# Kernel optimization log

Hardware: AMD Instinct MI355X
Metric: run time of the kernel (lower is better)

The kernel has to match this reference:

```python
import jax, jax.numpy as jnp
import numpy as np

EPS = 1e-9


def _feature_map(x, W, b):
    # nn.Linear: x @ W.T + b, then concat[exp(z), exp(-z)] on last dim
    z = jnp.einsum('bnd,ed->bne', x, W) + b
    return jnp.concatenate([jnp.exp(z), jnp.exp(-z)], axis=-1)  # [b, n, 2d]


def setup_inputs() -> dict:
    key = jax.random.key(0)
    ks = jax.random.split(key, 6)
    b, n, d = 4, 4096, 64
    s = 1.0 / np.sqrt(d)
    hidden = jax.random.normal(ks[0], (b, n, d), dtype=jnp.float32)
    # Hedgehog init is identity + zero bias; add tiny noise so grads are generic
    eye = jnp.eye(d, dtype=jnp.float32)
    Wq_mlp = eye + 0.02 * jax.random.normal(ks[1], (d, d), dtype=jnp.float32)
    Wk_mlp = eye + 0.02 * jax.random.normal(ks[2], (d, d), dtype=jnp.float32)
    bq_mlp = jnp.zeros((d,), dtype=jnp.float32)
    bk_mlp = jnp.zeros((d,), dtype=jnp.float32)
    Wq_base = s * jax.random.normal(ks[3], (d, d), dtype=jnp.float32)
    Wk_base = s * jax.random.normal(ks[4], (d, d), dtype=jnp.float32)
    return {"hidden_states": hidden, "Wq_mlp": Wq_mlp, "bq_mlp": bq_mlp,
            "Wk_mlp": Wk_mlp, "bk_mlp": bk_mlp,
            "Wq_base": Wq_base, "Wk_base": Wk_base}


def reference(hidden_states, Wq_mlp, bq_mlp, Wk_mlp, bk_mlp, Wq_base, Wk_base):
    d = hidden_states.shape[-1]
    # frozen base attention -> true_attn [b, n, n]
    qb = jnp.einsum('bnd,ed->bne', hidden_states, Wq_base)
    kb = jnp.einsum('bnd,ed->bne', hidden_states, Wk_base)
    true_attn = jax.nn.softmax(
        jnp.einsum('bmd,bnd->bmn', qb, kb) / jnp.sqrt(jnp.float32(d)), axis=-1)
    # hedgehog feature maps -> [b, n, 2d]
    q = _feature_map(hidden_states, Wq_mlp, bq_mlp)
    k = _feature_map(hidden_states, Wk_mlp, bk_mlp)
    # quadratic scores + softmax (note: linear-attention form is NOT used here)
    scores = jnp.einsum('bmd,bnd->bmn', q, k)
    pred_attn = jax.nn.softmax(scores, axis=-1)
    # soft-label cross entropy (KD loss)
    loss = jnp.mean(jnp.sum(-true_attn * jnp.log(pred_attn + EPS), axis=-1))
    return (loss, pred_attn, true_attn)
```

## Files before the change

kernel.cpp:

```cpp
#include <hip/hip_runtime.h>
#include <hip/hip_bf16.h>
#include <math.h>


#define B 4
#define N 4096
#define D 64
#define NROWS (B * N)
#define ATTN_ELEMS ((size_t)B * N * N)
#define FSTAT_BASE 12582912

typedef __attribute__((ext_vector_type(8))) short short8;
typedef __attribute__((ext_vector_type(4))) float float4v;

typedef unsigned short ushort_t;

__device__ __forceinline__ float fast_exp(float x) { return __expf(x); }
__device__ __forceinline__ float fast_log(float x) { return __logf(x); }

__device__ __forceinline__ void split_bf16(float x, ushort_t& hi, ushort_t& lo) {
  __hip_bfloat16 h = __float2bfloat16(x);
  float r = x - __bfloat162float(h);
  __hip_bfloat16 l = __float2bfloat16(r);
  hi = *(ushort_t*)&h;
  lo = *(ushort_t*)&l;
}

__device__ __forceinline__ void gload_lds16(const ushort_t* g, ushort_t* l) {
  __builtin_amdgcn_global_load_lds(
      (const __attribute__((address_space(1))) unsigned int*)g,
      (__attribute__((address_space(3))) unsigned int*)l, 16, 0, 0);
}

__device__ __forceinline__ float block_reduce(float v, bool is_max, float* red) {
#pragma unroll
  for (int o = 32; o > 0; o >>= 1) {
    float other = __shfl_down(v, o);
    v = is_max ? fmaxf(v, other) : (v + other);
  }
  int w = threadIdx.x >> 6;
  __syncthreads();
  if ((threadIdx.x & 63) == 0) red[w] = v;
  __syncthreads();
  return is_max ? fmaxf(fmaxf(red[0], red[1]), fmaxf(red[2], red[3]))
                : (red[0] + red[1] + red[2] + red[3]);
}

#define PR 32

__global__ __launch_bounds__(256, 2) void proj_kernel(
    const float* __restrict__ hidden,
    const float* __restrict__ Wq_mlp, const float* __restrict__ bq_mlp,
    const float* __restrict__ Wk_mlp, const float* __restrict__ bk_mlp,
    const float* __restrict__ Wq_base, const float* __restrict__ Wk_base,
    ushort_t* __restrict__ ws) {
  ushort_t* qbh = ws;
  ushort_t* qbl = ws + 1048576;
  ushort_t* kbh = ws + 2097152;
  ushort_t* kbl = ws + 3145728;
  ushort_t* qfh = ws + 4194304;
  ushort_t* qfl = ws + 6291456;
  ushort_t* kfh = ws + 8388608;
  ushort_t* kfl = ws + 10485760;

  __shared__ float wt[4][64 * 64];
  __shared__ float hs[PR][64];

  const int tid = threadIdx.x;
  const int r0 = blockIdx.x * PR;

  {
    const float* Wm[4] = {Wq_base, Wk_base, Wq_mlp, Wk_mlp};
#pragma unroll
    for (int m = 0; m < 4; ++m)
      for (int idx = tid; idx < 4096; idx += 256) {
        const int e = idx >> 6, d = idx & 63;
        wt[m][d * 64 + (e ^ (d & 31))] = Wm[m][idx];
      }
  }
  for (int idx = tid; idx < PR * 64; idx += 256)
    hs[idx >> 6][idx & 63] = hidden[(size_t)r0 * 64 + idx];
  __syncthreads();

  const int e = tid & 63;
  const int g0 = (tid >> 6) * (PR / 4);

  float aqb[PR / 4], akb[PR / 4], zq[PR / 4], zk[PR / 4];
  const float bq = bq_mlp[e], bk = bk_mlp[e];
#pragma unroll
  for (int g = 0; g < PR / 4; ++g) {
    aqb[g] = 0.f; akb[g] = 0.f; zq[g] = bq; zk[g] = bk;
  }

#pragma unroll 8
  for (int d = 0; d < 64; ++d) {
    const int wi = d * 64 + (e ^ (d & 31));
    const float w0 = wt[0][wi];
    const float w1 = wt[1][wi];
    const float w2 = wt[2][wi];
    const float w3 = wt[3][wi];
#pragma unroll
    for (int g = 0; g < PR / 4; ++g) {
      const float hd = hs[g0 + g][d];
      aqb[g] += hd * w0;
      akb[g] += hd * w1;
      zq[g] += hd * w2;
      zk[g] += hd * w3;
    }
  }

#pragma unroll
  for (int g = 0; g < PR / 4; ++g) {
    const int row = r0 + g0 + g;
    const size_t rb = (size_t)row * D + e;
    const size_t rf = (size_t)row * 2 * D + e;
    ushort_t hi, lo;
    split_bf16(aqb[g], hi, lo);        qbh[rb] = hi; qbl[rb] = lo;
    split_bf16(akb[g], hi, lo);        kbh[rb] = hi; kbl[rb] = lo;
    split_bf16(expf(zq[g]), hi, lo);   qfh[rf] = hi; qfl[rf] = lo;
    split_bf16(expf(-zq[g]), hi, lo);  qfh[rf + D] = hi; qfl[rf + D] = lo;
    split_bf16(expf(zk[g]), hi, lo);   kfh[rf] = hi; kfl[rf] = lo;
    split_bf16(expf(-zk[g]), hi, lo);  kfh[rf + D] = hi; kfl[rf + D] = lo;
  }
}

__global__ __launch_bounds__(256) void stats_kernel(
    const ushort_t* __restrict__ ws, float* __restrict__ fst) {
  const ushort_t* qbh = ws;
  const ushort_t* qbl = ws + 1048576;
  const ushort_t* kbh = ws + 2097152;
  const ushort_t* kbl = ws + 3145728;
  const ushort_t* qfh = ws + 4194304;
  const ushort_t* qfl = ws + 6291456;
  const ushort_t* kfh = ws + 8388608;
  const ushort_t* kfl = ws + 10485760;

  float* mt_ = fst;
  float* ist_ = fst + 16384;
  float* mp_ = fst + 32768;
  float* isp_ = fst + 49152;

  __shared__ ushort_t sbh[128 * 64];
  __shared__ ushort_t sbl[128 * 64];
  __shared__ ushort_t sfh[128 * 128];
  __shared__ ushort_t sfl[128 * 128];

  const int bid0 = blockIdx.x;
  const int bid = (bid0 & 7) * 32 + (bid0 >> 3);
  const int bt = bid >> 6;
  const int m0 = (bid & 63) * 64;
  const int tid = threadIdx.x;
  const int w = tid >> 6;
  const int lane = tid & 63;
  const int fr = lane & 15;
  const int quad = lane >> 4;
  const size_t rowb = (size_t)bt * N;

  const size_t ar = rowb + m0 + w * 16 + fr;
  short8 ath[2], atl[2], aph[4], apl[4];
#pragma unroll
  for (int kk = 0; kk < 2; ++kk) {
    ath[kk] = *(const short8*)&qbh[ar * 64 + kk * 32 + quad * 8];
    atl[kk] = *(const short8*)&qbl[ar * 64 + kk * 32 + quad * 8];
  }
#pragma unroll
  for (int kk = 0; kk < 4; ++kk) {
    aph[kk] = *(const short8*)&qfh[ar * 128 + kk * 32 + quad * 8];
    apl[kk] = *(const short8*)&qfl[ar * 128 + kk * 32 + quad * 8];
  }

  const int sr8 = lane >> 3, su8 = (lane & 7) ^ (lane >> 3);
  const int r4 = lane >> 4, u16 = lane & 15;

  float m_t[4], s_t[4], m_p[4], s_p[4];
#pragma unroll
  for (int r = 0; r < 4; ++r) {
    m_t[r] = -INFINITY; s_t[r] = 0.f;
    m_p[r] = -INFINITY; s_p[r] = 0.f;
  }

  for (int c = 0; c < 32; ++c) {
    const int n0 = c * 128;
    __syncthreads();
#pragma unroll
    for (int j = 0; j < 4; ++j) {
      const int g = j * 4 + w;
      const size_t grow = rowb + n0 + g * 8 + sr8;
      gload_lds16(kbh + grow * 64 + su8 * 8, &sbh[g * 512]);
      gload_lds16(kbl + grow * 64 + su8 * 8, &sbl[g * 512]);
    }
#pragma unroll
    for (int j = 0; j < 8; ++j) {
      const int g = j * 4 + w;
      const int su = u16 ^ ((g & 1) * 4 + r4);
      const size_t grow = rowb + n0 + g * 4 + r4;
      gload_lds16(kfh + grow * 128 + su * 8, &sfh[g * 512]);
      gload_lds16(kfl + grow * 128 + su * 8, &sfl[g * 512]);
    }
    __syncthreads();

    float4v acct[8];
#pragma unroll
    for (int tn = 0; tn < 8; ++tn) acct[tn] = (float4v)0.f;
#pragma unroll
    for (int tn = 0; tn < 8; ++tn) {
      const int brow = tn * 16 + fr;
#pragma unroll
      for (int kk = 0; kk < 2; ++kk) {
        const int u = ((kk * 4 + quad) ^ (fr & 7)) * 8;
        short8 bh = *(const short8*)&sbh[brow * 64 + u];
        short8 bl = *(const short8*)&sbl[brow * 64 + u];
        acct[tn] = __builtin_amdgcn_mfma_f32_16x16x32_bf16(ath[kk], bh, acct[tn], 0, 0, 0);
        acct[tn] = __builtin_amdgcn_mfma_f32_16x16x32_bf16(ath[kk], bl, acct[tn], 0, 0, 0);
        acct[tn] = __builtin_amdgcn_mfma_f32_16x16x32_bf16(atl[kk], bh, acct[tn], 0, 0, 0);
      }
    }
#pragma unroll
    for (int r = 0; r < 4; ++r) {
      float vm = m_t[r];
      float v[8];
#pragma unroll
      for (int tn = 0; tn < 8; ++tn) { v[tn] = acct[tn][r] * 0.125f; vm = fmaxf(vm, v[tn]); }
      float ss = s_t[r] * fast_exp(m_t[r] - vm);
#pragma unroll
      for (int tn = 0; tn < 8; ++tn) ss += fast_exp(v[tn] - vm);
      m_t[r] = vm; s_t[r] = ss;
    }

    float4v accp[8];
#pragma unroll
    for (int tn = 0; tn < 8; ++tn) accp[tn] = (float4v)0.f;
#pragma unroll
    for (int tn = 0; tn < 8; ++tn) {
      const int brow = tn * 16 + fr;
#pragma unroll
      for (int kk = 0; kk < 4; ++kk) {
        const int u = ((kk * 4 + quad) ^ (fr & 7)) * 8;
        short8 bh = *(const short8*)&sfh[brow * 128 + u];
        short8 bl = *(const short8*)&sfl[brow * 128 + u];
        accp[tn] = __builtin_amdgcn_mfma_f32_16x16x32_bf16(aph[kk], bh, accp[tn], 0, 0, 0);
        accp[tn] = __builtin_amdgcn_mfma_f32_16x16x32_bf16(aph[kk], bl, accp[tn], 0, 0, 0);
        accp[tn] = __builtin_amdgcn_mfma_f32_16x16x32_bf16(apl[kk], bh, accp[tn], 0, 0, 0);
      }
    }
#pragma unroll
    for (int r = 0; r < 4; ++r) {
      float vm = m_p[r];
      float v[8];
#pragma unroll
      for (int tn = 0; tn < 8; ++tn) { v[tn] = accp[tn][r]; vm = fmaxf(vm, v[tn]); }
      float ss = s_p[r] * fast_exp(m_p[r] - vm);
#pragma unroll
      for (int tn = 0; tn < 8; ++tn) ss += fast_exp(v[tn] - vm);
      m_p[r] = vm; s_p[r] = ss;
    }
  }

#pragma unroll
  for (int r = 0; r < 4; ++r) {
    {
      float m = m_t[r], s = s_t[r];
#pragma unroll
      for (int o = 1; o < 16; o <<= 1) {
        float m2 = __shfl_xor(m, o);
        float s2 = __shfl_xor(s, o);
        float M = fmaxf(m, m2);
        s = s * fast_exp(m - M) + s2 * fast_exp(m2 - M);
        m = M;
      }
      if (fr == 0) {
        const size_t row = rowb + m0 + w * 16 + quad * 4 + r;
        mt_[row] = m; ist_[row] = 1.f / s;
      }
    }
    {
      float m = m_p[r], s = s_p[r];
#pragma unroll
      for (int o = 1; o < 16; o <<= 1) {
        float m2 = __shfl_xor(m, o);
        float s2 = __shfl_xor(s, o);
        float M = fmaxf(m, m2);
        s = s * fast_exp(m - M) + s2 * fast_exp(m2 - M);
        m = M;
      }
      if (fr == 0) {
        const size_t row = rowb + m0 + w * 16 + quad * 4 + r;
        mp_[row] = m; isp_[row] = 1.f / s;
      }
    }
  }
}

__global__ __launch_bounds__(256, 2) void scores_write_kernel(
    const ushort_t* __restrict__ ws, float* __restrict__ out,
    float* __restrict__ fst) {
  const ushort_t* qbh = ws;
  const ushort_t* qbl = ws + 1048576;
  const ushort_t* kbh = ws + 2097152;
  const ushort_t* kbl = ws + 3145728;
  const ushort_t* qfh = ws + 4194304;
  const ushort_t* qfl = ws + 6291456;
  const ushort_t* kfh = ws + 8388608;
  const ushort_t* kfl = ws + 10485760;

  const float* mt_ = fst;
  const float* ist_ = fst + 16384;
  const float* mp_ = fst + 32768;
  const float* isp_ = fst + 49152;
  float* partials = fst + 65536;

  __shared__ ushort_t sAh[128 * 64];
  __shared__ ushort_t sAl[128 * 64];
  __shared__ ushort_t sBh[128 * 64];
  __shared__ ushort_t sBl[128 * 64];
  __shared__ float red[4];

  const int bt = blockIdx.z;
  const int f = blockIdx.x + 32 * blockIdx.y;
  const int nf = (f & 7) * 128 + (f >> 3);
  const int m0 = (nf >> 5) * 128;
  const int n0 = (nf & 31) * 128;

  const int tid = threadIdx.x;
  const int lane = tid & 63;
  const int w = tid >> 6;
  const int qr = w >> 1, qc = w & 1;
  const int fr = lane & 15;
  const int quad = lane >> 4;

  const int srow = lane >> 3;
  const int sunit = (lane & 7) ^ srow;

  const size_t rowb = (size_t)bt * N;
  float* pred = out + 1;
  float* tru  = out + 1 + ATTN_ELEMS;

  float4v tsave[4][4];
  float lloss = 0.f;

#pragma unroll
  for (int phase = 0; phase < 2; ++phase) {
    const ushort_t* Ah = phase ? qfh : qbh;
    const ushort_t* Al = phase ? qfl : qbl;
    const ushort_t* Bh = phase ? kfh : kbh;
    const ushort_t* Bl = phase ? kfl : kbl;
    const int Krow = phase ? 128 : 64;
    const int nchunk = Krow / 64;
    const float scale = phase ? 1.0f : 0.125f;
    float* dst = phase ? pred : tru;

    float4v acc[4][4];
#pragma unroll
    for (int i = 0; i < 4; ++i)
#pragma unroll
      for (int j = 0; j < 4; ++j) acc[i][j] = (float4v)0.f;

    for (int ck = 0; ck < nchunk; ++ck) {
      const int kc = ck * 64;
      __syncthreads();
#pragma unroll
      for (int j = 0; j < 4; ++j) {
        const int chunk = j * 4 + w;
        const int r = chunk * 8 + srow;
        const int loff = chunk * 512;
        const size_t gA = (size_t)(rowb + m0 + r) * Krow + kc + sunit * 8;
        const size_t gB = (size_t)(rowb + n0 + r) * Krow + kc + sunit * 8;
        gload_lds16(Ah + gA, &sAh[loff]);
        gload_lds16(Al + gA, &sAl[loff]);
        gload_lds16(Bh + gB, &sBh[loff]);
        gload_lds16(Bl + gB, &sBl[loff]);
      }
      __syncthreads();

#pragma unroll
      for (int kk = 0; kk < 2; ++kk) {
        short8 ah[4], al[4], bh[4], bl[4];
        const int u8 = ((kk * 4 + quad) ^ (fr & 7)) * 8;
#pragma unroll
        for (int t = 0; t < 4; ++t) {
          const int offA = (qr * 64 + t * 16 + fr) * 64 + u8;
          const int offB = (qc * 64 + t * 16 + fr) * 64 + u8;
          ah[t] = *(const short8*)&sAh[offA];
          al[t] = *(const short8*)&sAl[offA];
          bh[t] = *(const short8*)&sBh[offB];
          bl[t] = *(const short8*)&sBl[offB];
        }
#pragma unroll
        for (int tm = 0; tm < 4; ++tm)
#pragma unroll
          for (int tn = 0; tn < 4; ++tn) {
            acc[tm][tn] = __builtin_amdgcn_mfma_f32_16x16x32_bf16(
                ah[tm], bh[tn], acc[tm][tn], 0, 0, 0);
            acc[tm][tn] = __builtin_amdgcn_mfma_f32_16x16x32_bf16(
                ah[tm], bl[tn], acc[tm][tn], 0, 0, 0);
            acc[tm][tn] = __builtin_amdgcn_mfma_f32_16x16x32_bf16(
                al[tm], bh[tn], acc[tm][tn], 0, 0, 0);
          }
      }
    }

#pragma unroll
    for (int tm = 0; tm < 4; ++tm) {
      const int rbase = m0 + qr * 64 + tm * 16 + quad * 4;
      float mrow[4], isrow[4];
#pragma unroll
      for (int reg = 0; reg < 4; ++reg) {
        const size_t gr = rowb + rbase + reg;
        mrow[reg]  = phase ? mp_[gr]  : mt_[gr];
        isrow[reg] = phase ? isp_[gr] : ist_[gr];
      }
#pragma unroll
      for (int tn = 0; tn < 4; ++tn) {
        const int c = n0 + qc * 64 + tn * 16 + fr;
        float4v v = acc[tm][tn];
        float4v pv;
#pragma unroll
        for (int reg = 0; reg < 4; ++reg)
          pv[reg] = fast_exp(v[reg] * scale - mrow[reg]) * isrow[reg];
#pragma unroll
        for (int reg = 0; reg < 4; ++reg)
          dst[(rowb + rbase + reg) * N + c] = pv[reg];
        if (phase == 0) {
          tsave[tm][tn] = pv;
        } else {
#pragma unroll
          for (int reg = 0; reg < 4; ++reg)
            lloss -= tsave[tm][tn][reg] * fast_log(pv[reg] + 1e-9f);
        }
      }
    }
  }

  lloss = block_reduce(lloss, false, red);
  if (tid == 0) partials[f + (bt << 10)] = lloss;
}

__global__ __launch_bounds__(256) void reduce_loss_kernel(
    const float* __restrict__ partials, float* __restrict__ out) {
  const int tid = threadIdx.x;
  __shared__ float red[4];
  float s = 0.f;
  for (int i = tid; i < 4096; i += 256) s += partials[i];
  s = block_reduce(s, false, red);
  if (tid == 0) out[0] = s * (1.0f / (float)NROWS);
}

extern "C" void kernel_launch(void* const* d_in, const int* in_sizes, int n_in,
                              void* d_out, int out_size, void* d_ws, size_t ws_size,
                              hipStream_t stream) {
  const float* hidden  = (const float*)d_in[0];
  const float* Wq_mlp  = (const float*)d_in[1];
  const float* bq_mlp  = (const float*)d_in[2];
  const float* Wk_mlp  = (const float*)d_in[3];
  const float* bk_mlp  = (const float*)d_in[4];
  const float* Wq_base = (const float*)d_in[5];
  const float* Wk_base = (const float*)d_in[6];
  float* out = (float*)d_out;
  ushort_t* ws = (ushort_t*)d_ws;
  float* fst = (float*)(ws + FSTAT_BASE);

  proj_kernel<<<NROWS / PR, 256, 0, stream>>>(hidden, Wq_mlp, bq_mlp, Wk_mlp,
                                              bk_mlp, Wq_base, Wk_base, ws);
  stats_kernel<<<256, 256, 0, stream>>>(ws, fst);
  scores_write_kernel<<<dim3(32, 32, B), 256, 0, stream>>>(ws, out, fst);
  reduce_loss_kernel<<<1, 256, 0, stream>>>(fst + 65536, out);
}
```

Before: 787.3 us.

## Double-buffer B tiles, read A from global, pack saved true_attn to bf16

The scores kernel stops staging the A (query) operands in shared memory and reads its A fragments straight from global memory into registers. It double-buffers the B (key) tiles so the next chunk's async load overlaps the current MFMA work and the true_attn epilogue. The true_attn values kept for the loss are packed into bf16 pairs, halving that register footprint. This lowers LDS traffic and register pressure, at the cost of uncoalesced direct global A loads and a small precision loss in the loss term.

```diff
diff --git a/kernel.cpp b/kernel.cpp
--- a/kernel.cpp
+++ b/kernel.cpp
@@ -24,6 +24,16 @@
   __hip_bfloat16 l = __float2bfloat16(r);
   hi = *(ushort_t*)&h;
   lo = *(ushort_t*)&l;
+}
+
+__device__ __forceinline__ unsigned int pack_bf16(float a, float b) {
+  __hip_bfloat16 ha = __float2bfloat16(a);
+  __hip_bfloat16 hb = __float2bfloat16(b);
+  return (unsigned int)(*(ushort_t*)&ha) | ((unsigned int)(*(ushort_t*)&hb) << 16);
+}
+__device__ __forceinline__ float unpack_bf16(unsigned int u, int hi) {
+  unsigned int bits = hi ? (u & 0xffff0000u) : (u << 16);
+  return *(float*)&bits;
 }
 
 __device__ __forceinline__ void gload_lds16(const ushort_t* g, ushort_t* l) {
@@ -309,10 +319,8 @@
   const float* isp_ = fst + 49152;
   float* partials = fst + 65536;
 
-  __shared__ ushort_t sAh[128 * 64];
-  __shared__ ushort_t sAl[128 * 64];
-  __shared__ ushort_t sBh[128 * 64];
-  __shared__ ushort_t sBl[128 * 64];
+  __shared__ ushort_t sBh[2][128 * 64];
+  __shared__ ushort_t sBl[2][128 * 64];
   __shared__ float red[4];
 
   const int bt = blockIdx.z;
@@ -332,102 +340,128 @@
   const int sunit = (lane & 7) ^ srow;
 
   const size_t rowb = (size_t)bt * N;
+  const size_t arow = rowb + m0 + qr * 64 + fr;
   float* pred = out + 1;
   float* tru  = out + 1 + ATTN_ELEMS;
 
-  float4v tsave[4][4];
+  auto stageB = [&](int buf, const ushort_t* Bh, const ushort_t* Bl,
+                    int Krow, int kc) {
+#pragma unroll
+    for (int j = 0; j < 4; ++j) {
+      const int chunk = j * 4 + w;
+      const int r = chunk * 8 + srow;
+      const size_t gB = (size_t)(rowb + n0 + r) * Krow + kc + sunit * 8;
+      gload_lds16(Bh + gB, &sBh[buf][chunk * 512]);
+      gload_lds16(Bl + gB, &sBl[buf][chunk * 512]);
+    }
+  };
+
+  auto computeChunk = [&](int buf, const ushort_t* Ah, const ushort_t* Al,
+                          int Krow, int kc, float4v (&acc)[4][4]) {
+#pragma unroll
+    for (int kk = 0; kk < 2; ++kk) {
+      short8 ah[4], al[4], bh[4], bl[4];
+#pragma unroll
+      for (int t = 0; t < 4; ++t) {
+        const size_t ga = (arow + t * 16) * Krow + kc + kk * 32 + quad * 8;
+        ah[t] = *(const short8*)&Ah[ga];
+        al[t] = *(const short8*)&Al[ga];
+      }
+      const int u8 = ((kk * 4 + quad) ^ (fr & 7)) * 8;
+#pragma unroll
+      for (int t = 0; t < 4; ++t) {
+        const int offB = (qc * 64 + t * 16 + fr) * 64 + u8;
+        bh[t] = *(const short8*)&sBh[buf][offB];
+        bl[t] = *(const short8*)&sBl[buf][offB];
+      }
+#pragma unroll
+      for (int tm = 0; tm < 4; ++tm)
+#pragma unroll
+        for (int tn = 0; tn < 4; ++tn) {
+          acc[tm][tn] = __builtin_amdgcn_mfma_f32_16x16x32_bf16(
+              ah[tm], bh[tn], acc[tm][tn], 0, 0, 0);
+          acc[tm][tn] = __builtin_amdgcn_mfma_f32_16x16x32_bf16(
+              ah[tm], bl[tn], acc[tm][tn], 0, 0, 0);
+          acc[tm][tn] = __builtin_amdgcn_mfma_f32_16x16x32_bf16(
+              al[tm], bh[tn], acc[tm][tn], 0, 0, 0);
+        }
+    }
+  };
+
   float lloss = 0.f;
-
-#pragma unroll
-  for (int phase = 0; phase < 2; ++phase) {
-    const ushort_t* Ah = phase ? qfh : qbh;
-    const ushort_t* Al = phase ? qfl : qbl;
-    const ushort_t* Bh = phase ? kfh : kbh;
-    const ushort_t* Bl = phase ? kfl : kbl;
-    const int Krow = phase ? 128 : 64;
-    const int nchunk = Krow / 64;
-    const float scale = phase ? 1.0f : 0.125f;
-    float* dst = phase ? pred : tru;
-
-    float4v acc[4][4];
-#pragma unroll
-    for (int i = 0; i < 4; ++i)
-#pragma unroll
-      for (int j = 0; j < 4; ++j) acc[i][j] = (float4v)0.f;
-
-    for (int ck = 0; ck < nchunk; ++ck) {
-      const int kc = ck * 64;
-      __syncthreads();
-#pragma unroll
-      for (int j = 0; j < 4; ++j) {
-        const int chunk = j * 4 + w;
-        const int r = chunk * 8 + srow;
-        const int loff = chunk * 512;
-        const size_t gA = (size_t)(rowb + m0 + r) * Krow + kc + sunit * 8;
-        const size_t gB = (size_t)(rowb + n0 + r) * Krow + kc + sunit * 8;
-        gload_lds16(Ah + gA, &sAh[loff]);
-        gload_lds16(Al + gA, &sAl[loff]);
-        gload_lds16(Bh + gB, &sBh[loff]);
-        gload_lds16(Bl + gB, &sBl[loff]);
-      }
-      __syncthreads();
-
-#pragma unroll
-      for (int kk = 0; kk < 2; ++kk) {
-        short8 ah[4], al[4], bh[4], bl[4];
-        const int u8 = ((kk * 4 + quad) ^ (fr & 7)) * 8;
-#pragma unroll
-        for (int t = 0; t < 4; ++t) {
-          const int offA = (qr * 64 + t * 16 + fr) * 64 + u8;
-          const int offB = (qc * 64 + t * 16 + fr) * 64 + u8;
-          ah[t] = *(const short8*)&sAh[offA];
-          al[t] = *(const short8*)&sAl[offA];
-          bh[t] = *(const short8*)&sBh[offB];
-          bl[t] = *(const short8*)&sBl[offB];
-        }
-#pragma unroll
-        for (int tm = 0; tm < 4; ++tm)
-#pragma unroll
-          for (int tn = 0; tn < 4; ++tn) {
-            acc[tm][tn] = __builtin_amdgcn_mfma_f32_16x16x32_bf16(
-                ah[tm], bh[tn], acc[tm][tn], 0, 0, 0);
-            acc[tm][tn] = __builtin_amdgcn_mfma_f32_16x16x32_bf16(
-                ah[tm], bl[tn], acc[tm][tn], 0, 0, 0);
-            acc[tm][tn] = __builtin_amdgcn_mfma_f32_16x16x32_bf16(
-                al[tm], bh[tn], acc[tm][tn], 0, 0, 0);
-          }
-      }
-    }
-
-#pragma unroll
-    for (int tm = 0; tm < 4; ++tm) {
-      const int rbase = m0 + qr * 64 + tm * 16 + quad * 4;
-      float mrow[4], isrow[4];
-#pragma unroll
-      for (int reg = 0; reg < 4; ++reg) {
-        const size_t gr = rowb + rbase + reg;
-        mrow[reg]  = phase ? mp_[gr]  : mt_[gr];
-        isrow[reg] = phase ? isp_[gr] : ist_[gr];
-      }
-#pragma unroll
-      for (int tn = 0; tn < 4; ++tn) {
-        const int c = n0 + qc * 64 + tn * 16 + fr;
-        float4v v = acc[tm][tn];
-        float4v pv;
-#pragma unroll
-        for (int reg = 0; reg < 4; ++reg)
-          pv[reg] = fast_exp(v[reg] * scale - mrow[reg]) * isrow[reg];
-#pragma unroll
-        for (int reg = 0; reg < 4; ++reg)
-          dst[(rowb + rbase + reg) * N + c] = pv[reg];
-        if (phase == 0) {
-          tsave[tm][tn] = pv;
-        } else {
-#pragma unroll
-          for (int reg = 0; reg < 4; ++reg)
-            lloss -= tsave[tm][tn][reg] * fast_log(pv[reg] + 1e-9f);
-        }
-      }
+  unsigned int tsp[4][4][2];
+
+  float4v acc[4][4];
+#pragma unroll
+  for (int i = 0; i < 4; ++i)
+#pragma unroll
+    for (int j = 0; j < 4; ++j) acc[i][j] = (float4v)0.f;
+
+  stageB(0, kbh, kbl, 64, 0);
+  __syncthreads();
+  computeChunk(0, qbh, qbl, 64, 0, acc);
+  stageB(1, kfh, kfl, 128, 0);
+
+#pragma unroll
+  for (int tm = 0; tm < 4; ++tm) {
+    const int rbase = m0 + qr * 64 + tm * 16 + quad * 4;
+    float mrow[4], isrow[4];
+#pragma unroll
+    for (int reg = 0; reg < 4; ++reg) {
+      const size_t gr = rowb + rbase + reg;
+      mrow[reg] = mt_[gr]; isrow[reg] = ist_[gr];
+    }
+#pragma unroll
+    for (int tn = 0; tn < 4; ++tn) {
+      const int c = n0 + qc * 64 + tn * 16 + fr;
+      float4v v = acc[tm][tn];
+      float4v pv;
+#pragma unroll
+      for (int reg = 0; reg < 4; ++reg)
+        pv[reg] = fast_exp(v[reg] * 0.125f - mrow[reg]) * isrow[reg];
+#pragma unroll
+      for (int reg = 0; reg < 4; ++reg)
+        tru[(rowb + rbase + reg) * N + c] = pv[reg];
+      tsp[tm][tn][0] = pack_bf16(pv[0], pv[1]);
+      tsp[tm][tn][1] = pack_bf16(pv[2], pv[3]);
+    }
+  }
+  __syncthreads();
+
+#pragma unroll
+  for (int i = 0; i < 4; ++i)
+#pragma unroll
+    for (int j = 0; j < 4; ++j) acc[i][j] = (float4v)0.f;
+
+  stageB(0, kfh, kfl, 128, 64);
+  computeChunk(1, qfh, qfl, 128, 0, acc);
+  __syncthreads();
+  computeChunk(0, qfh, qfl, 128, 64, acc);
+
+#pragma unroll
+  for (int tm = 0; tm < 4; ++tm) {
+    const int rbase = m0 + qr * 64 + tm * 16 + quad * 4;
+    float mrow[4], isrow[4];
+#pragma unroll
+    for (int reg = 0; reg < 4; ++reg) {
+      const size_t gr = rowb + rbase + reg;
+      mrow[reg] = mp_[gr]; isrow[reg] = isp_[gr];
+    }
+#pragma unroll
+    for (int tn = 0; tn < 4; ++tn) {
+      const int c = n0 + qc * 64 + tn * 16 + fr;
+      float4v v = acc[tm][tn];
+      float4v pv;
+#pragma unroll
+      for (int reg = 0; reg < 4; ++reg)
+        pv[reg] = fast_exp(v[reg] - mrow[reg]) * isrow[reg];
+#pragma unroll
+      for (int reg = 0; reg < 4; ++reg)
+        pred[(rowb + rbase + reg) * N + c] = pv[reg];
+      lloss -= unpack_bf16(tsp[tm][tn][0], 0) * fast_log(pv[0] + 1e-9f);
+      lloss -= unpack_bf16(tsp[tm][tn][0], 1) * fast_log(pv[1] + 1e-9f);
+      lloss -= unpack_bf16(tsp[tm][tn][1], 0) * fast_log(pv[2] + 1e-9f);
+      lloss -= unpack_bf16(tsp[tm][tn][1], 1) * fast_log(pv[3] + 1e-9f);
     }
   }
 
```

Result: no change. 802.8 us (+2.0%).
